# Optimization experiments

Measured on AMD Instinct MI355X. Metric: run time of the kernel, lower is better.

Reference implementation:

```python
import jax, jax.numpy as jnp
import numpy as np

V, C, D = 25, 64, 64          # joints, in_channels, out_channels
N, T = 64, 300                # batch, frames
WEIGHT = 2
GROUPS = [[0, 12], [13, 24]]
BN_EPS = 1e-5


def _inner_shift(A, graph_group, node, channels, weight):
    """Faithful numpy port of Modified_grouped_shift_gcn.inner_shift."""
    index_array = np.arange(node * channels).reshape(node, channels)
    copy = index_array.copy()
    for grp in graph_group:
        lb, ub = int(np.min(grp)), int(np.max(grp)) + 1
        for i in range(lb, ub):
            cur = A[i].copy()
            cur[i] = 0
            neighbors = np.nonzero(cur)[0]
            j = 0
            ci = i - lb + 1
            while j < channels:
                nxt = ci % (ub - lb) + lb
                if j < weight:
                    j += weight
                elif nxt == i:
                    j += weight
                    ci += 1
                elif nxt in neighbors:
                    index_array[i][j:j + weight] = copy[nxt][j:j + weight]
                    j += weight
                    ci += 1
                else:
                    index_array[i][j] = copy[nxt][j]
                    j += 1
                    ci += 1
    return index_array.flatten()


def _adjacency():
    # chain skeleton with self loops, binarized as in __init__
    A = np.zeros((V, V), dtype=np.float64)
    for i in range(V - 1):
        A[i, i + 1] = 1.0
        A[i + 1, i] = 1.0
    np.fill_diagonal(A, 1.0)
    return A


def setup_inputs() -> dict:
    key = jax.random.key(0)
    k0, k1, k2, k3 = jax.random.split(key, 4)
    A = _adjacency()
    shift_in = jnp.asarray(_inner_shift(A, GROUPS, V, C, WEIGHT), dtype=jnp.int32)
    shift_out = jnp.asarray(_inner_shift(A, GROUPS, V, D, WEIGHT), dtype=jnp.int32)
    x0 = jax.random.normal(k0, (N, C, T, V), dtype=jnp.float32)
    feature_mask = 0.1 * jax.random.normal(k1, (1, V, C), dtype=jnp.float32)
    W = jax.random.normal(k2, (C, D), dtype=jnp.float32) * np.float32(np.sqrt(1.0 / D))
    b = 0.01 * jax.random.normal(k3, (1, 1, D), dtype=jnp.float32)
    gamma = jnp.ones((V * D,), dtype=jnp.float32)
    beta = jnp.zeros((V * D,), dtype=jnp.float32)
    return {"x0": x0, "feature_mask": feature_mask, "W": W, "b": b,
            "gamma": gamma, "beta": beta,
            "shift_in": shift_in, "shift_out": shift_out}


def reference(x0, feature_mask, W, b, gamma, beta, shift_in, shift_out):
    n, c, t, v = x0.shape
    # (n, c, t, v) -> (n*t, v*c)
    x = jnp.transpose(x0, (0, 2, 3, 1)).reshape(n * t, v * c)
    # channel-wise shift gather (precomputed permutation)
    x = x[:, shift_in].reshape(n * t, v, c)
    # learned feature mask
    x = x * (jnp.tanh(feature_mask) + 1.0)
    # pointwise linear + bias
    x = jnp.einsum('nvc,cd->nvd', x, W) + b
    x = x.reshape(n * t, v * W.shape[1])
    # second shift gather
    x = x[:, shift_out]
    # BatchNorm1d, training mode (biased batch stats)
    mean = jnp.mean(x, axis=0)
    var = jnp.var(x, axis=0)
    x = (x - mean) * jax.lax.rsqrt(var + BN_EPS) * gamma + beta
    # back to (n, d, t, v), residual (in==out so down is identity), relu
    x = x.reshape(n, t, v, W.shape[1]).transpose(0, 3, 1, 2)
    return jax.nn.relu(x + x0)
```

## Files before the change

kernel.cpp:

```cpp
#include <hip/hip_runtime.h>
#include <math.h>

#define V_ 25
#define C_ 64
#define D_ 64
#define N_ 64
#define T_ 300
#define R_ (N_*T_)
#define K_ (V_*C_)
#define BN_EPS 1e-5f

#define WS_GM    0
#define WS_SUM   1600
#define WS_SQ    3200
#define WS_WBF   4800
#define WS_SC2   6848
#define WS_SH2   13248
#define WS_YO    19648

#define P1_GRID  512
#define NWIN     4800

using bf16x8 = __attribute__((ext_vector_type(8))) short;
using f32x4  = __attribute__((ext_vector_type(4))) float;
using i32x4  = __attribute__((ext_vector_type(4))) int;

__device__ __forceinline__ unsigned short f2bf(float f) {
    unsigned u = __float_as_uint(f);
    return (unsigned short)((u + 0x7FFFu + ((u >> 16) & 1u)) >> 16);
}

__device__ __forceinline__ void gload16(const void* g, void* l) {
    __builtin_amdgcn_global_load_lds(
        (const __attribute__((address_space(1))) void*)g,
        (__attribute__((address_space(3))) void*)l, 16, 0, 0);
}

__device__ __forceinline__ void barrier_lds() {
    asm volatile("s_waitcnt lgkmcnt(0)" ::: "memory");
    __builtin_amdgcn_sched_barrier(0);
    __builtin_amdgcn_s_barrier();
    __builtin_amdgcn_sched_barrier(0);
}

__global__ __launch_bounds__(256) void prep_tables(
    const float* __restrict__ fm, const float* __restrict__ W,
    const int* __restrict__ s_in, float* __restrict__ ws)
{
    int idx = blockIdx.x * 256 + threadIdx.x;
    if (idx < K_) {
        int jj  = s_in[idx];
        int off = (jj & 63) * 100 + (jj >> 6);
        unsigned mk = (unsigned)f2bf(tanhf(fm[idx]) + 1.0f);
        ((unsigned*)ws)[WS_GM + idx] = (mk << 16) | (unsigned)off;
    }
    if (idx < C_ * D_) ((unsigned short*)(ws + WS_WBF))[idx] = f2bf(W[idx]);
}

__global__ __launch_bounds__(256) void stats_reduce(
    const float* __restrict__ pbuf, float* __restrict__ ws)
{
    __shared__ float red[256];
    int jq = threadIdx.x & 15;
    int bq = threadIdx.x >> 4;
    int j  = blockIdx.x * 16 + jq;
    const float* p = pbuf + (size_t)(bq * 32) * 3200 + j;
    float s = 0.f;
    #pragma unroll 8
    for (int k = 0; k < 32; ++k)
        s += p[(size_t)k * 3200];
    red[threadIdx.x] = s;
    __syncthreads();
    if (bq < 8) red[threadIdx.x] += red[threadIdx.x + 128];
    __syncthreads();
    if (bq < 4) red[threadIdx.x] += red[threadIdx.x + 64];
    __syncthreads();
    if (bq < 2) red[threadIdx.x] += red[threadIdx.x + 32];
    __syncthreads();
    if (bq == 0) ws[WS_SUM + j] = red[jq] + red[jq + 16];
}

__global__ __launch_bounds__(256) void prep_scale_kernel(
    const float* __restrict__ gamma, const float* __restrict__ beta,
    const int* __restrict__ s_out, float* __restrict__ ws)
{
    int e = blockIdx.x * 256 + threadIdx.x;
    if (e < 6400) {
        int dd  = e / 100;
        int rem = e - dd * 100;
        int dt  = rem / 25;
        int v   = rem - dt * 25;
        int k   = v * 64 + dd;
        int jj  = s_out[k];
        float mean = ws[WS_SUM + jj] * (1.0f / (float)R_);
        float var  = fmaf(-mean, mean, ws[WS_SQ + jj] * (1.0f / (float)R_));
        float inv  = rsqrtf(var + BN_EPS);
        float sc   = gamma[k] * inv;
        ws[WS_SC2 + e] = sc;
        ws[WS_SH2 + e] = beta[k] - mean * sc;
        ((unsigned*)ws)[WS_YO + e] = (unsigned)((jj & 63) * 100 + dt * 25 + (jj >> 6));
    }
}

__device__ __forceinline__ const float* win_ptr(const float* x0, int wi) {
    int r0 = wi * 4;
    int n  = r0 / 300;
    int t0 = r0 - n * 300;
    return x0 + (size_t)n * 480000 + t0 * 25;
}

__device__ __forceinline__ void issue_stage(
    const float* __restrict__ xwin, float4* dst, const int gOff[7], int tid)
{
    const float4* s4 = (const float4*)xwin;
    #pragma unroll
    for (int i = 0; i < 7; ++i) {
        int idx = i * 256 + tid;
        if (idx < 1600)
            gload16(s4 + gOff[i], dst + idx);
    }
}

__device__ __forceinline__ void load_gmr(
    const unsigned* __restrict__ gmt, unsigned gmr[28], int lane, int w)
{
    int jw = lane & 3;
    int vh = lane >> 4;
    #pragma unroll
    for (int i = 0; i < 14; ++i) {
        int combo = i * 4 + w;
        int T  = combo >> 2;
        int q2 = combo & 3;
        int t  = T >> 1;
        int c0 = (T & 1) * 32 + q2 * 8 + jw * 2;
        int v  = t * 4 + vh;
        int kb = (v < V_) ? (v * 64 + c0) : c0;
        gmr[2 * i]     = gmt[kb];
        gmr[2 * i + 1] = gmt[kb + 1];
    }
}

__device__ __forceinline__ void build_afm(
    const float* xs, unsigned* a_fm32, const unsigned gmr[28], int lane, int w)
{
    int m  = lane >> 2;
    int jw = lane & 3;
    int dt = m & 3;
    #pragma unroll
    for (int i = 0; i < 14; ++i) {
        int combo = i * 4 + w;
        int T  = combo >> 2;
        int q2 = combo & 3;
        unsigned g0 = gmr[2 * i], g1 = gmr[2 * i + 1];
        float m0 = __uint_as_float(g0 & 0xFFFF0000u);
        float m1 = __uint_as_float(g1 & 0xFFFF0000u);
        float f0 = xs[(g0 & 0xFFFFu) + dt * 25] * m0;
        float f1 = xs[(g1 & 0xFFFFu) + dt * 25] * m1;
        a_fm32[(T * 64 + q2 * 16 + m) * 4 + jw] =
            (unsigned)f2bf(f0) | ((unsigned)f2bf(f1) << 16);
    }
}

__global__ __launch_bounds__(256) void pass1_stats(
    const float* __restrict__ x0, const float* __restrict__ bg,
    const float* __restrict__ ws, float* __restrict__ pbuf)
{
    __shared__ __align__(16) float4 xs2[2][1600];
    __shared__ __align__(16) unsigned a_fm32[3584];
    const bf16x8* afp = (const bf16x8*)a_fm32;

    int tid = threadIdx.x;
    int lane = tid & 63, w = tid >> 6;
    int l15 = lane & 15, q = lane >> 4;
    int d = w * 16 + l15;

    const unsigned short* Wbf = (const unsigned short*)(ws + WS_WBF);
    bf16x8 bfrag0, bfrag1;
    #pragma unroll
    for (int j = 0; j < 8; ++j) {
        bfrag0[j] = (short)Wbf[(q * 8 + j) * 64 + d];
        bfrag1[j] = (short)Wbf[(32 + q * 8 + j) * 64 + d];
    }
    float breg = bg[d];

    unsigned gmr[28];
    load_gmr((const unsigned*)ws + WS_GM, gmr, lane, w);

    int gOff[7];
    #pragma unroll
    for (int i = 0; i < 7; ++i) {
        int idx = i * 256 + tid;
        int c = idx / 25;
        int r = idx - c * 25;
        gOff[i] = c * 1875 + r;
    }

    float sums[7], sqs[7];
    #pragma unroll
    for (int t = 0; t < 7; ++t) { sums[t] = 0.f; sqs[t] = 0.f; }

    int wi = blockIdx.x;
    issue_stage(win_ptr(x0, wi), xs2[0], gOff, tid);
    int cur = 0;

    while (true) {
        __syncthreads();
        int nwi = wi + P1_GRID;
        if (nwi < NWIN)
            issue_stage(win_ptr(x0, nwi), xs2[cur ^ 1], gOff, tid);

        build_afm((const float*)xs2[cur], a_fm32, gmr, lane, w);
        barrier_lds();

        #pragma unroll
        for (int t = 0; t < 7; ++t) {
            bf16x8 a0 = afp[(t * 2 + 0) * 64 + lane];
            bf16x8 a1 = afp[(t * 2 + 1) * 64 + lane];
            f32x4 acc = {0.f, 0.f, 0.f, 0.f};
            acc = __builtin_amdgcn_mfma_f32_16x16x32_bf16(a0, bfrag0, acc, 0, 0, 0);
            acc = __builtin_amdgcn_mfma_f32_16x16x32_bf16(a1, bfrag1, acc, 0, 0, 0);
            #pragma unroll
            for (int r = 0; r < 4; ++r) {
                float y = acc[r] + breg;
                sums[t] += y;
                sqs[t]   = fmaf(y, y, sqs[t]);
            }
        }
        if (nwi >= NWIN) break;
        wi = nwi; cur ^= 1;
    }

    float* pout = pbuf + (size_t)blockIdx.x * 3200;
    #pragma unroll
    for (int t = 0; t < 7; ++t) {
        int v = t * 4 + q;
        if (v < V_) {
            __builtin_nontemporal_store(sums[t], &pout[v * 64 + d]);
            __builtin_nontemporal_store(sqs[t],  &pout[1600 + v * 64 + d]);
        }
    }
}

__global__ __launch_bounds__(256, 3) void pass2_out(
    const float* __restrict__ x0, const float* __restrict__ bg,
    const float* __restrict__ ws, float* __restrict__ out)
{
    __shared__ __align__(16) float4 xs4[1600];
    __shared__ __align__(16) float  yu[6400];
    const float* xs = (const float*)xs4;
    unsigned* a_fm32 = (unsigned*)yu;
    const bf16x8* afp = (const bf16x8*)yu;
    float* y_lds = yu;

    int tid = threadIdx.x;
    int lane = tid & 63, w = tid >> 6;
    int l15 = lane & 15, q = lane >> 4;
    int d = w * 16 + l15;

    int r0 = blockIdx.x * 4;
    int n  = r0 / 300;
    int t0 = r0 - n * 300;

    int gOff[7];
    #pragma unroll
    for (int i = 0; i < 7; ++i) {
        int idx = i * 256 + tid;
        int c = idx / 25;
        int r = idx - c * 25;
        gOff[i] = c * 1875 + r;
    }
    issue_stage(x0 + (size_t)n * 480000 + t0 * 25, xs4, gOff, tid);

    const unsigned short* Wbf = (const unsigned short*)(ws + WS_WBF);
    bf16x8 bfrag0, bfrag1;
    #pragma unroll
    for (int j = 0; j < 8; ++j) {
        bfrag0[j] = (short)Wbf[(q * 8 + j) * 64 + d];
        bfrag1[j] = (short)Wbf[(32 + q * 8 + j) * 64 + d];
    }
    float breg = bg[d];
    unsigned gmr[28];
    load_gmr((const unsigned*)ws + WS_GM, gmr, lane, w);

    __syncthreads();
    build_afm(xs, a_fm32, gmr, lane, w);
    __syncthreads();

    bf16x8 af[14];
    #pragma unroll
    for (int t2 = 0; t2 < 14; ++t2)
        af[t2] = afp[t2 * 64 + lane];
    __syncthreads();

    #pragma unroll
    for (int t = 0; t < 7; ++t) {
        f32x4 acc = {0.f, 0.f, 0.f, 0.f};
        acc = __builtin_amdgcn_mfma_f32_16x16x32_bf16(af[2 * t],     bfrag0, acc, 0, 0, 0);
        acc = __builtin_amdgcn_mfma_f32_16x16x32_bf16(af[2 * t + 1], bfrag1, acc, 0, 0, 0);
        int v = t * 4 + q;
        if (v < V_) {
            #pragma unroll
            for (int r = 0; r < 4; ++r)
                y_lds[d * 100 + r * 25 + v] = acc[r] + breg;
        }
    }
    __syncthreads();

    const f32x4* sc4 = (const f32x4*)(ws + WS_SC2);
    const f32x4* sh4 = (const f32x4*)(ws + WS_SH2);
    const i32x4* yo4 = (const i32x4*)((const int*)ws + WS_YO);
    const f32x4* rs4 = (const f32x4*)xs;
    float* outbase = out + (size_t)n * 480000 + t0 * 25;
    #pragma unroll
    for (int i = 0; i < 7; ++i) {
        int idx = i * 256 + tid;
        if (idx < 1600) {
            int dd  = idx / 25;
            int pos = idx - dd * 25;
            f32x4 sc = sc4[idx];
            f32x4 sh = sh4[idx];
            i32x4 yo = yo4[idx];
            f32x4 rs = rs4[idx];
            f32x4 o;
            o[0] = fmaxf(fmaf(y_lds[yo[0]], sc[0], sh[0]) + rs[0], 0.f);
            o[1] = fmaxf(fmaf(y_lds[yo[1]], sc[1], sh[1]) + rs[1], 0.f);
            o[2] = fmaxf(fmaf(y_lds[yo[2]], sc[2], sh[2]) + rs[2], 0.f);
            o[3] = fmaxf(fmaf(y_lds[yo[3]], sc[3], sh[3]) + rs[3], 0.f);
            __builtin_nontemporal_store(o, (f32x4*)(outbase + dd * 7500) + pos);
        }
    }
}

extern "C" void kernel_launch(void* const* d_in, const int* in_sizes, int n_in,
                              void* d_out, int out_size, void* d_ws, size_t ws_size,
                              hipStream_t stream)
{
    const float* x0    = (const float*)d_in[0];
    const float* fm    = (const float*)d_in[1];
    const float* W     = (const float*)d_in[2];
    const float* b     = (const float*)d_in[3];
    const float* gamma = (const float*)d_in[4];
    const float* beta  = (const float*)d_in[5];
    const int*   s_in  = (const int*)d_in[6];
    const int*   s_out = (const int*)d_in[7];
    float* out = (float*)d_out;
    float* ws  = (float*)d_ws;

    prep_tables<<<16, 256, 0, stream>>>(fm, W, s_in, ws);
    pass1_stats<<<P1_GRID, 256, 0, stream>>>(x0, b, ws, out);
    stats_reduce<<<200, 256, 0, stream>>>(out, ws);
    prep_scale_kernel<<<25, 256, 0, stream>>>(gamma, beta, s_out, ws);
    pass2_out<<<NWIN, 256, 0, stream>>>(x0, b, ws, out);
}
```

Measured before the change: 273.0 us.

## Make pass2 persistent with prefetch, hoist bias from stats loop, use packed bf16 convert

Pass2 now runs a persistent grid of 768 blocks that loop over windows. It prefetches the next window into LDS right after building the A fragments, and re-reads the residual from global memory because the LDS buffer has been overwritten. Pass1 accumulates raw MFMA outputs and folds the bias into the sum and sum-of-squares once at the end. build_afm uses the v_cvt_pk_bf16_f32 instruction instead of manual rounding. The costs are an extra global read of the residual in pass2, and the bias fold computes the sums in a different order, which can shift float rounding slightly.

Result: slower. 328.0 us (+20.1%).

```diff
diff --git a/kernel.cpp b/kernel.cpp
--- a/kernel.cpp
+++ b/kernel.cpp
@@ -19,6 +19,7 @@
 #define WS_YO    19648
 
 #define P1_GRID  512
+#define P2_GRID  768
 #define NWIN     4800
 
 using bf16x8 = __attribute__((ext_vector_type(8))) short;
@@ -28,6 +29,12 @@
 __device__ __forceinline__ unsigned short f2bf(float f) {
     unsigned u = __float_as_uint(f);
     return (unsigned short)((u + 0x7FFFu + ((u >> 16) & 1u)) >> 16);
+}
+
+__device__ __forceinline__ unsigned cvt_pk_bf16(float lo, float hi) {
+    unsigned r;
+    asm("v_cvt_pk_bf16_f32 %0, %1, %2" : "=v"(r) : "v"(lo), "v"(hi));
+    return r;
 }
 
 __device__ __forceinline__ void gload16(const void* g, void* l) {
@@ -156,8 +163,7 @@
         float m1 = __uint_as_float(g1 & 0xFFFF0000u);
         float f0 = xs[(g0 & 0xFFFFu) + dt * 25] * m0;
         float f1 = xs[(g1 & 0xFFFFu) + dt * 25] * m1;
-        a_fm32[(T * 64 + q2 * 16 + m) * 4 + jw] =
-            (unsigned)f2bf(f0) | ((unsigned)f2bf(f1) << 16);
+        a_fm32[(T * 64 + q2 * 16 + m) * 4 + jw] = cvt_pk_bf16(f0, f1);
     }
 }
 
@@ -200,6 +206,7 @@
     for (int t = 0; t < 7; ++t) { sums[t] = 0.f; sqs[t] = 0.f; }
 
     int wi = blockIdx.x;
+    int wcount = 0;
     issue_stage(win_ptr(x0, wi), xs2[0], gOff, tid);
     int cur = 0;
 
@@ -211,6 +218,7 @@
 
         build_afm((const float*)xs2[cur], a_fm32, gmr, lane, w);
         barrier_lds();
+        ++wcount;
 
         #pragma unroll
         for (int t = 0; t < 7; ++t) {
@@ -221,22 +229,24 @@
             acc = __builtin_amdgcn_mfma_f32_16x16x32_bf16(a1, bfrag1, acc, 0, 0, 0);
             #pragma unroll
             for (int r = 0; r < 4; ++r) {
-                float y = acc[r] + breg;
-                sums[t] += y;
-                sqs[t]   = fmaf(y, y, sqs[t]);
+                sums[t] += acc[r];
+                sqs[t]   = fmaf(acc[r], acc[r], sqs[t]);
             }
         }
         if (nwi >= NWIN) break;
         wi = nwi; cur ^= 1;
     }
 
+    float nb = 4.0f * (float)wcount;
     float* pout = pbuf + (size_t)blockIdx.x * 3200;
     #pragma unroll
     for (int t = 0; t < 7; ++t) {
         int v = t * 4 + q;
         if (v < V_) {
-            __builtin_nontemporal_store(sums[t], &pout[v * 64 + d]);
-            __builtin_nontemporal_store(sqs[t],  &pout[1600 + v * 64 + d]);
+            float qf = fmaf(2.0f * breg, sums[t], fmaf(nb * breg, breg, sqs[t]));
+            float sf = fmaf(nb, breg, sums[t]);
+            __builtin_nontemporal_store(sf, &pout[v * 64 + d]);
+            __builtin_nontemporal_store(qf, &pout[1600 + v * 64 + d]);
         }
     }
 }
@@ -257,10 +267,6 @@
     int l15 = lane & 15, q = lane >> 4;
     int d = w * 16 + l15;
 
-    int r0 = blockIdx.x * 4;
-    int n  = r0 / 300;
-    int t0 = r0 - n * 300;
-
     int gOff[7];
     #pragma unroll
     for (int i = 0; i < 7; ++i) {
@@ -269,7 +275,7 @@
         int r = idx - c * 25;
         gOff[i] = c * 1875 + r;
     }
-    issue_stage(x0 + (size_t)n * 480000 + t0 * 25, xs4, gOff, tid);
+    issue_stage(win_ptr(x0, blockIdx.x), xs4, gOff, tid);
 
     const unsigned short* Wbf = (const unsigned short*)(ws + WS_WBF);
     bf16x8 bfrag0, bfrag1;
@@ -282,52 +288,65 @@
     unsigned gmr[28];
     load_gmr((const unsigned*)ws + WS_GM, gmr, lane, w);
 
-    __syncthreads();
-    build_afm(xs, a_fm32, gmr, lane, w);
-    __syncthreads();
-
-    bf16x8 af[14];
-    #pragma unroll
-    for (int t2 = 0; t2 < 14; ++t2)
-        af[t2] = afp[t2 * 64 + lane];
-    __syncthreads();
-
-    #pragma unroll
-    for (int t = 0; t < 7; ++t) {
-        f32x4 acc = {0.f, 0.f, 0.f, 0.f};
-        acc = __builtin_amdgcn_mfma_f32_16x16x32_bf16(af[2 * t],     bfrag0, acc, 0, 0, 0);
-        acc = __builtin_amdgcn_mfma_f32_16x16x32_bf16(af[2 * t + 1], bfrag1, acc, 0, 0, 0);
-        int v = t * 4 + q;
-        if (v < V_) {
-            #pragma unroll
-            for (int r = 0; r < 4; ++r)
-                y_lds[d * 100 + r * 25 + v] = acc[r] + breg;
-        }
-    }
-    __syncthreads();
-
     const f32x4* sc4 = (const f32x4*)(ws + WS_SC2);
     const f32x4* sh4 = (const f32x4*)(ws + WS_SH2);
     const i32x4* yo4 = (const i32x4*)((const int*)ws + WS_YO);
-    const f32x4* rs4 = (const f32x4*)xs;
-    float* outbase = out + (size_t)n * 480000 + t0 * 25;
-    #pragma unroll
-    for (int i = 0; i < 7; ++i) {
-        int idx = i * 256 + tid;
-        if (idx < 1600) {
-            int dd  = idx / 25;
-            int pos = idx - dd * 25;
-            f32x4 sc = sc4[idx];
-            f32x4 sh = sh4[idx];
-            i32x4 yo = yo4[idx];
-            f32x4 rs = rs4[idx];
-            f32x4 o;
-            o[0] = fmaxf(fmaf(y_lds[yo[0]], sc[0], sh[0]) + rs[0], 0.f);
-            o[1] = fmaxf(fmaf(y_lds[yo[1]], sc[1], sh[1]) + rs[1], 0.f);
-            o[2] = fmaxf(fmaf(y_lds[yo[2]], sc[2], sh[2]) + rs[2], 0.f);
-            o[3] = fmaxf(fmaf(y_lds[yo[3]], sc[3], sh[3]) + rs[3], 0.f);
-            __builtin_nontemporal_store(o, (f32x4*)(outbase + dd * 7500) + pos);
+
+    int wi = blockIdx.x;
+    while (true) {
+        __syncthreads();
+        build_afm(xs, a_fm32, gmr, lane, w);
+        __syncthreads();
+
+        int nwi = wi + P2_GRID;
+        if (nwi < NWIN)
+            issue_stage(win_ptr(x0, nwi), xs4, gOff, tid);
+
+        bf16x8 af[14];
+        #pragma unroll
+        for (int t2 = 0; t2 < 14; ++t2)
+            af[t2] = afp[t2 * 64 + lane];
+        barrier_lds();
+
+        #pragma unroll
+        for (int t = 0; t < 7; ++t) {
+            f32x4 acc = {0.f, 0.f, 0.f, 0.f};
+            acc = __builtin_amdgcn_mfma_f32_16x16x32_bf16(af[2 * t],     bfrag0, acc, 0, 0, 0);
+            acc = __builtin_amdgcn_mfma_f32_16x16x32_bf16(af[2 * t + 1], bfrag1, acc, 0, 0, 0);
+            int v = t * 4 + q;
+            if (v < V_) {
+                #pragma unroll
+                for (int r = 0; r < 4; ++r)
+                    y_lds[d * 100 + r * 25 + v] = acc[r] + breg;
+            }
         }
+        barrier_lds();
+
+        int r0 = wi * 4;
+        int n  = r0 / 300;
+        int t0 = r0 - n * 300;
+        float* outbase = out + (size_t)n * 480000 + t0 * 25;
+        const float* inbase = x0 + (size_t)n * 480000 + t0 * 25;
+        #pragma unroll
+        for (int i = 0; i < 7; ++i) {
+            int idx = i * 256 + tid;
+            if (idx < 1600) {
+                int dd  = idx / 25;
+                int pos = idx - dd * 25;
+                f32x4 sc = sc4[idx];
+                f32x4 sh = sh4[idx];
+                i32x4 yo = yo4[idx];
+                f32x4 rs = ((const f32x4*)(inbase + dd * 7500))[pos];
+                f32x4 o;
+                o[0] = fmaxf(fmaf(y_lds[yo[0]], sc[0], sh[0]) + rs[0], 0.f);
+                o[1] = fmaxf(fmaf(y_lds[yo[1]], sc[1], sh[1]) + rs[1], 0.f);
+                o[2] = fmaxf(fmaf(y_lds[yo[2]], sc[2], sh[2]) + rs[2], 0.f);
+                o[3] = fmaxf(fmaf(y_lds[yo[3]], sc[3], sh[3]) + rs[3], 0.f);
+                __builtin_nontemporal_store(o, (f32x4*)(outbase + dd * 7500) + pos);
+            }
+        }
+        if (nwi >= NWIN) break;
+        wi = nwi;
     }
 }
 
@@ -350,5 +369,5 @@
     pass1_stats<<<P1_GRID, 256, 0, stream>>>(x0, b, ws, out);
     stats_reduce<<<200, 256, 0, stream>>>(out, ws);
     prep_scale_kernel<<<25, 256, 0, stream>>>(gamma, beta, s_out, ws);
-    pass2_out<<<NWIN, 256, 0, stream>>>(x0, b, ws, out);
-}
+    pass2_out<<<P2_GRID, 256, 0, stream>>>(x0, b, ws, out);
+}
```
